# Kernel optimization log

Measured on AMD Instinct MI355X. Metric: run time of the kernel, lower is better.

Reference implementation:

```python
import jax, jax.numpy as jnp
import numpy as np

N = 50000   # nodes
D = 128     # hidden_channels
E = 625000  # edges (before self-loops)
NEG_SLOPE = 0.2


def setup_inputs() -> dict:
    key = jax.random.key(0)
    ks = jax.random.split(key, 10)
    s = 1.0 / np.sqrt(D)
    return {
        "x": jax.random.normal(ks[0], (N, D), dtype=jnp.float32),
        "edge_index": jax.random.randint(ks[1], (2, E), 0, N, dtype=jnp.int64),
        "W1": jax.random.normal(ks[2], (D, D), dtype=jnp.float32) * s,
        "a_src1": jax.random.normal(ks[3], (D,), dtype=jnp.float32) * s,
        "a_dst1": jax.random.normal(ks[4], (D,), dtype=jnp.float32) * s,
        "b1": jax.random.normal(ks[5], (D,), dtype=jnp.float32) * 0.01,
        "W2": jax.random.normal(ks[6], (D, D), dtype=jnp.float32) * s,
        "a_src2": jax.random.normal(ks[7], (D,), dtype=jnp.float32) * s,
        "a_dst2": jax.random.normal(ks[8], (D,), dtype=jnp.float32) * s,
        "b2": jax.random.normal(ks[9], (D,), dtype=jnp.float32) * 0.01,
    }


def gat_layer(x, src, dst, W, a_src, a_dst, b):
    # x: [N, D]; src/dst: [E'] (self-loops already appended)
    h = x @ W                                   # [N, D]
    s_src = h @ a_src                           # [N]
    s_dst = h @ a_dst                           # [N]
    e = s_src[src] + s_dst[dst]                 # [E'] per-edge logits
    e = jnp.where(e > 0, e, NEG_SLOPE * e)      # leaky_relu
    # softmax over incoming edges of each dst node (self-loops -> no empty segments)
    m = jax.ops.segment_max(e, dst, num_segments=N)
    p = jnp.exp(e - m[dst])
    z = jax.ops.segment_sum(p, dst, num_segments=N)
    alpha = p / (z[dst] + 1e-16)                # [E']
    out = jax.ops.segment_sum(alpha[:, None] * h[src], dst, num_segments=N)
    return out + b


def reference(x, edge_index, W1, a_src1, a_dst1, b1, W2, a_src2, a_dst2, b2):
    loop = jnp.arange(N, dtype=edge_index.dtype)
    src = jnp.concatenate([edge_index[0], loop])
    dst = jnp.concatenate([edge_index[1], loop])
    h = jax.nn.relu(gat_layer(x, src, dst, W1, a_src1, a_dst1, b1))
    return gat_layer(h, src, dst, W2, a_src2, a_dst2, b2)
```

## Files before the change

kernel.cpp:

```cpp
#include <hip/hip_runtime.h>
#include <hip/hip_fp16.h>

#define D 128
#define NEG_SLOPE 0.2f


__global__ __launch_bounds__(256) void partial_kernel(const int* __restrict__ deg,
                                                      int* __restrict__ psum, int N) {
  __shared__ int s[256];
  int t = threadIdx.x;
  int i = blockIdx.x * 256 + t;
  s[t] = (i < N) ? deg[i] : 0;
  __syncthreads();
  #pragma unroll
  for (int o = 128; o; o >>= 1) { if (t < o) s[t] += s[t + o]; __syncthreads(); }
  if (t == 0) psum[blockIdx.x] = s[0];
}

__global__ __launch_bounds__(1024) void scan_partials(const int* __restrict__ psum,
                                                      int* __restrict__ bbase,
                                                      int* __restrict__ off, int NB, int N) {
  __shared__ int s[1024];
  int t = threadIdx.x;
  int v = (t < NB) ? psum[t] : 0;
  s[t] = v;
  __syncthreads();
  for (int o = 1; o < 1024; o <<= 1) {
    int u = (t >= o) ? s[t - o] : 0;
    __syncthreads();
    s[t] += u;
    __syncthreads();
  }
  if (t < NB) bbase[t] = s[t] - v;
  if (t == 1023) off[N] = s[1023];
}

__global__ __launch_bounds__(256) void offs_kernel(const int* __restrict__ deg,
                                                   const int* __restrict__ bbase,
                                                   int* __restrict__ off, int N) {
  __shared__ int s[256];
  int t = threadIdx.x;
  int i = blockIdx.x * 256 + t;
  int v = (i < N) ? deg[i] : 0;
  s[t] = v;
  __syncthreads();
  #pragma unroll
  for (int o = 1; o < 256; o <<= 1) {
    int u = (t >= o) ? s[t - o] : 0;
    __syncthreads();
    s[t] += u;
    __syncthreads();
  }
  if (i < N) off[i] = bbase[blockIdx.x] + s[t] - v;
}

__global__ __launch_bounds__(256) void scatter_kernel(
    const int* __restrict__ src, const int* __restrict__ dst,
    const int* __restrict__ rank, int E, int N,
    const int* __restrict__ off, int* __restrict__ csr) {
  int i = blockIdx.x * blockDim.x + threadIdx.x;
  if (i >= E + N) return;
  int s, d;
  if (i < E) { s = src[i]; d = dst[i]; } else { s = i - E; d = s; }
  csr[off[d] + rank[i]] = s;
}


__global__ __launch_bounds__(256, 2) void gemm_hist_fused(
    const float* __restrict__ X, const float* __restrict__ W,
    const float* __restrict__ avs, const float* __restrict__ avd,
    __half* __restrict__ H, float* __restrict__ Ss, float* __restrict__ Sd, int N,
    const int* __restrict__ dstE, int E, int* __restrict__ deg, int* __restrict__ rank,
    int nbGemm, int nbHist)
{
  if (blockIdx.x >= nbGemm) {
    if (dstE == nullptr) return;
    int b = blockIdx.x - nbGemm;
    int EP = E + N;
    int stride = nbHist * 256;
    for (int i = b * 256 + (int)threadIdx.x; i < EP; i += stride) {
      int d = (i < E) ? dstE[i] : (i - E);
      rank[i] = atomicAdd(&deg[d], 1);
    }
    return;
  }

  __shared__ float At[32 * 68];
  __shared__ float Ws[32 * 128];
  int tid = threadIdx.x;
  int tx = tid & 15, ty = tid >> 4;
  int row0 = blockIdx.x * 64;

  float acc[4][8];
  #pragma unroll
  for (int i = 0; i < 4; ++i)
    #pragma unroll
    for (int j = 0; j < 8; ++j) acc[i][j] = 0.f;

  float as_[8], ad_[8];
  #pragma unroll
  for (int j = 0; j < 4; ++j) {
    as_[j]     = avs[tx * 4 + j];      ad_[j]     = avd[tx * 4 + j];
    as_[j + 4] = avs[64 + tx * 4 + j]; ad_[j + 4] = avd[64 + tx * 4 + j];
  }

  for (int kc = 0; kc < 4; ++kc) {
    #pragma unroll
    for (int it = 0; it < 4; ++it) {
      int lin = it * 256 + tid;
      int r = lin >> 4;
      int c2 = lin & 15;
      int gr = row0 + r;
      float2 v = make_float2(0.f, 0.f);
      if (gr < N) v = *(const float2*)&X[(size_t)gr * D + kc * 32 + c2 * 2];
      At[(c2 * 2) * 68 + r] = v.x;
      At[(c2 * 2 + 1) * 68 + r] = v.y;
    }
    #pragma unroll
    for (int it = 0; it < 4; ++it) {
      int lin = it * 256 + tid;
      int r = lin >> 5;
      int c4 = lin & 31;
      *(float4*)&Ws[r * 128 + c4 * 4] =
          *(const float4*)&W[(size_t)(kc * 32 + r) * D + c4 * 4];
    }
    __syncthreads();
    #pragma unroll 8
    for (int k = 0; k < 32; ++k) {
      float4 a0 = *(const float4*)&At[k * 68 + ty * 4];
      float4 w0 = *(const float4*)&Ws[k * 128 + tx * 4];
      float4 w1 = *(const float4*)&Ws[k * 128 + 64 + tx * 4];
      float a[4] = {a0.x, a0.y, a0.z, a0.w};
      float wv[8] = {w0.x, w0.y, w0.z, w0.w, w1.x, w1.y, w1.z, w1.w};
      #pragma unroll
      for (int i = 0; i < 4; ++i)
        #pragma unroll
        for (int j = 0; j < 8; ++j) acc[i][j] += a[i] * wv[j];
    }
    __syncthreads();
  }

  #pragma unroll
  for (int i = 0; i < 4; ++i) {
    int r = row0 + ty * 4 + i;
    bool ok = r < N;
    if (ok) {
      __half2 o0 = __floats2half2_rn(acc[i][0], acc[i][1]);
      __half2 o1 = __floats2half2_rn(acc[i][2], acc[i][3]);
      __half2 o2 = __floats2half2_rn(acc[i][4], acc[i][5]);
      __half2 o3 = __floats2half2_rn(acc[i][6], acc[i][7]);
      *(__half2*)&H[(size_t)r * D + tx * 4]          = o0;
      *(__half2*)&H[(size_t)r * D + tx * 4 + 2]      = o1;
      *(__half2*)&H[(size_t)r * D + 64 + tx * 4]     = o2;
      *(__half2*)&H[(size_t)r * D + 64 + tx * 4 + 2] = o3;
    }
    float ps = 0.f, pd = 0.f;
    #pragma unroll
    for (int j = 0; j < 8; ++j) { ps += acc[i][j] * as_[j]; pd += acc[i][j] * ad_[j]; }
    ps += __shfl_down(ps, 8); pd += __shfl_down(pd, 8);
    ps += __shfl_down(ps, 4); pd += __shfl_down(pd, 4);
    ps += __shfl_down(ps, 2); pd += __shfl_down(pd, 2);
    ps += __shfl_down(ps, 1); pd += __shfl_down(pd, 1);
    if (ok && tx == 0) { Ss[r] = ps; Sd[r] = pd; }
  }
}


__global__ __launch_bounds__(256) void agg_kernel(
    const __half* __restrict__ H, const float* __restrict__ Ssrc, const float* __restrict__ Sdst,
    const int* __restrict__ off, const int* __restrict__ csr, const float* __restrict__ bias,
    float* __restrict__ out, int N, int do_relu)
{
  int wid = threadIdx.x >> 6, lane = threadIdx.x & 63;
  int n = blockIdx.x * 4 + wid;
  if (n >= N) return;
  int st = off[n], en = off[n + 1];
  float sd = Sdst[n];

  float m = -1e30f;
  for (int j = st + lane; j < en; j += 64) {
    int s = csr[j];
    float e = Ssrc[s] + sd;
    e = e > 0.f ? e : NEG_SLOPE * e;
    m = fmaxf(m, e);
  }
  #pragma unroll
  for (int o = 32; o; o >>= 1) m = fmaxf(m, __shfl_xor(m, o));

  float z = 0.f, ax = 0.f, ay = 0.f;
  int c = lane * 2;
  for (int base = st; base < en; base += 64) {
    int j = base + lane;
    int cnt = min(64, en - base);
    float p = 0.f; int s = 0;
    if (j < en) {
      s = csr[j];
      float e = Ssrc[s] + sd;
      e = e > 0.f ? e : NEG_SLOPE * e;
      p = __expf(e - m);
    }
    z += p;
    for (int i = 0; i < cnt; i += 8) {
      float pu[8]; __half2 hv[8];
      #pragma unroll
      for (int u = 0; u < 8; ++u) {
        int idx = i + u;
        int iu = idx < cnt ? idx : cnt - 1;
        float pb = __shfl(p, iu);
        int   sb = __shfl(s, iu);
        pu[u] = idx < cnt ? pb : 0.f;
        hv[u] = *(const __half2*)&H[(size_t)sb * D + c];
      }
      #pragma unroll
      for (int u = 0; u < 8; ++u) {
        float2 f = __half22float2(hv[u]);
        ax += pu[u] * f.x; ay += pu[u] * f.y;
      }
    }
  }
  #pragma unroll
  for (int o = 32; o; o >>= 1) z += __shfl_xor(z, o);
  float inv = 1.f / (z + 1e-16f);
  float2 bv = *(const float2*)&bias[c];
  ax = ax * inv + bv.x;
  ay = ay * inv + bv.y;
  if (do_relu) { ax = fmaxf(ax, 0.f); ay = fmaxf(ay, 0.f); }
  *(float2*)&out[(size_t)n * D + c] = make_float2(ax, ay);
}


extern "C" void kernel_launch(void* const* d_in, const int* in_sizes, int n_in,
                              void* d_out, int out_size, void* d_ws, size_t ws_size,
                              hipStream_t stream) {
  const float* x   = (const float*)d_in[0];
  const int*   ei  = (const int*)d_in[1];
  const float* W1  = (const float*)d_in[2];
  const float* as1 = (const float*)d_in[3];
  const float* ad1 = (const float*)d_in[4];
  const float* b1  = (const float*)d_in[5];
  const float* W2  = (const float*)d_in[6];
  const float* as2 = (const float*)d_in[7];
  const float* ad2 = (const float*)d_in[8];
  const float* b2  = (const float*)d_in[9];

  int N  = in_sizes[0] / D;
  int E  = in_sizes[1] / 2;
  int EP = E + N;
  const int* src = ei;
  const int* dst = ei + E;

  char* w = (char*)d_ws;
  auto alloc = [&](size_t bytes) -> char* {
    char* p = w; w += (bytes + 511) & ~(size_t)511; return p;
  };
  int NB = (N + 255) / 256;
  int*    deg   = (int*)alloc((size_t)N * 4);
  int*    off   = (int*)alloc(((size_t)N + 1) * 4);
  int*    csr   = (int*)alloc((size_t)EP * 4);
  int*    rank  = (int*)alloc((size_t)EP * 4);
  int*    psum  = (int*)alloc((size_t)NB * 4);
  int*    bbase = (int*)alloc((size_t)NB * 4);
  float*  ssrc  = (float*)alloc((size_t)N * 4);
  float*  sdst  = (float*)alloc((size_t)N * 4);
  __half* h     = (__half*)alloc((size_t)N * D * 2);
  float*  t1    = (float*)alloc((size_t)N * D * 4);

  hipMemsetAsync(deg, 0, (size_t)N * 4, stream);

  int nbGemm = (N + 63) / 64;
  int nbHist = 1024;

  gemm_hist_fused<<<nbGemm + nbHist, 256, 0, stream>>>(
      x, W1, as1, ad1, h, ssrc, sdst, N, dst, E, deg, rank, nbGemm, nbHist);

  partial_kernel<<<NB, 256, 0, stream>>>(deg, psum, N);
  scan_partials<<<1, 1024, 0, stream>>>(psum, bbase, off, NB, N);
  offs_kernel<<<NB, 256, 0, stream>>>(deg, bbase, off, N);
  scatter_kernel<<<(EP + 255) / 256, 256, 0, stream>>>(src, dst, rank, E, N, off, csr);

  agg_kernel<<<(N + 3) / 4, 256, 0, stream>>>(h, ssrc, sdst, off, csr, b1, t1, N, 1);
  gemm_hist_fused<<<nbGemm, 256, 0, stream>>>(
      t1, W2, as2, ad2, h, ssrc, sdst, N, nullptr, 0, nullptr, nullptr, nbGemm, 0);
  agg_kernel<<<(N + 3) / 4, 256, 0, stream>>>(h, ssrc, sdst, off, csr, b2, (float*)d_out, N, 0);
}
```

Measured before the change: 244.4 us.

## Use fp16 MFMA for node projection and store intermediate activations in half

Result: no change. 247.3 us (+1.2%).

```diff
diff --git a/kernel.cpp b/kernel.cpp
--- a/kernel.cpp
+++ b/kernel.cpp
@@ -3,6 +3,10 @@
 
 #define D 128
 #define NEG_SLOPE 0.2f
+#define WT_STRIDE 136
+
+typedef __attribute__((ext_vector_type(8))) _Float16 v8h;
+typedef __attribute__((ext_vector_type(4))) float v4f;
 
 
 __global__ __launch_bounds__(256) void partial_kernel(const int* __restrict__ deg,
@@ -67,7 +71,8 @@
 
 
 __global__ __launch_bounds__(256, 2) void gemm_hist_fused(
-    const float* __restrict__ X, const float* __restrict__ W,
+    const float* __restrict__ Xf, const __half* __restrict__ Xh,
+    const float* __restrict__ W,
     const float* __restrict__ avs, const float* __restrict__ avd,
     __half* __restrict__ H, float* __restrict__ Ss, float* __restrict__ Sd, int N,
     const int* __restrict__ dstE, int E, int* __restrict__ deg, int* __restrict__ rank,
@@ -85,83 +90,77 @@
     return;
   }
 
-  __shared__ float At[32 * 68];
-  __shared__ float Ws[32 * 128];
+  __shared__ _Float16 Wt[128][WT_STRIDE];
+  __shared__ _Float16 wa[2][128];
+
   int tid = threadIdx.x;
-  int tx = tid & 15, ty = tid >> 4;
-  int row0 = blockIdx.x * 64;
-
-  float acc[4][8];
-  #pragma unroll
-  for (int i = 0; i < 4; ++i)
+
+  #pragma unroll
+  for (int it = 0; it < 16; ++it) {
+    int lin = it * 256 + tid;
+    int k  = lin >> 5;
+    int n4 = (lin & 31) * 4;
+    float4 v = *(const float4*)&W[(size_t)k * D + n4];
+    Wt[n4 + 0][k] = (_Float16)v.x;
+    Wt[n4 + 1][k] = (_Float16)v.y;
+    Wt[n4 + 2][k] = (_Float16)v.z;
+    Wt[n4 + 3][k] = (_Float16)v.w;
+  }
+  {
+    int k = tid & 127;
+    const float* vec = (tid < 128) ? avs : avd;
+    float s = 0.f;
+    #pragma unroll 8
+    for (int n = 0; n < 128; n += 4) {
+      float4 wv = *(const float4*)&W[(size_t)k * D + n];
+      float4 av = *(const float4*)&vec[n];
+      s += wv.x * av.x + wv.y * av.y + wv.z * av.z + wv.w * av.w;
+    }
+    wa[tid >> 7][k] = (_Float16)s;
+  }
+  __syncthreads();
+
+  int wid = tid >> 6, lane = tid & 63;
+  int quad = lane >> 4, nn = lane & 15;
+  int row = blockIdx.x * 64 + wid * 16 + nn;
+  int rowc = min(row, N - 1);
+
+  v4f acc[9];
+  #pragma unroll
+  for (int t = 0; t < 9; ++t) acc[t] = (v4f){0.f, 0.f, 0.f, 0.f};
+
+  #pragma unroll
+  for (int ks = 0; ks < 4; ++ks) {
+    int k0 = ks * 32 + quad * 8;
+    v8h b;
+    if (Xh) {
+      b = *(const v8h*)&Xh[(size_t)rowc * D + k0];
+    } else {
+      float4 x0 = *(const float4*)&Xf[(size_t)rowc * D + k0];
+      float4 x1 = *(const float4*)&Xf[(size_t)rowc * D + k0 + 4];
+      b[0] = (_Float16)x0.x; b[1] = (_Float16)x0.y;
+      b[2] = (_Float16)x0.z; b[3] = (_Float16)x0.w;
+      b[4] = (_Float16)x1.x; b[5] = (_Float16)x1.y;
+      b[6] = (_Float16)x1.z; b[7] = (_Float16)x1.w;
+    }
     #pragma unroll
-    for (int j = 0; j < 8; ++j) acc[i][j] = 0.f;
-
-  float as_[8], ad_[8];
-  #pragma unroll
-  for (int j = 0; j < 4; ++j) {
-    as_[j]     = avs[tx * 4 + j];      ad_[j]     = avd[tx * 4 + j];
-    as_[j + 4] = avs[64 + tx * 4 + j]; ad_[j + 4] = avd[64 + tx * 4 + j];
-  }
-
-  for (int kc = 0; kc < 4; ++kc) {
+    for (int t = 0; t < 8; ++t) {
+      v8h a = *(const v8h*)&Wt[t * 16 + nn][k0];
+      acc[t] = __builtin_amdgcn_mfma_f32_16x16x32_f16(a, b, acc[t], 0, 0, 0);
+    }
+    v8h awv = *(const v8h*)&wa[nn & 1][k0];
+    acc[8] = __builtin_amdgcn_mfma_f32_16x16x32_f16(awv, b, acc[8], 0, 0, 0);
+  }
+
+  if (row < N) {
     #pragma unroll
-    for (int it = 0; it < 4; ++it) {
-      int lin = it * 256 + tid;
-      int r = lin >> 4;
-      int c2 = lin & 15;
-      int gr = row0 + r;
-      float2 v = make_float2(0.f, 0.f);
-      if (gr < N) v = *(const float2*)&X[(size_t)gr * D + kc * 32 + c2 * 2];
-      At[(c2 * 2) * 68 + r] = v.x;
-      At[(c2 * 2 + 1) * 68 + r] = v.y;
-    }
-    #pragma unroll
-    for (int it = 0; it < 4; ++it) {
-      int lin = it * 256 + tid;
-      int r = lin >> 5;
-      int c4 = lin & 31;
-      *(float4*)&Ws[r * 128 + c4 * 4] =
-          *(const float4*)&W[(size_t)(kc * 32 + r) * D + c4 * 4];
-    }
-    __syncthreads();
-    #pragma unroll 8
-    for (int k = 0; k < 32; ++k) {
-      float4 a0 = *(const float4*)&At[k * 68 + ty * 4];
-      float4 w0 = *(const float4*)&Ws[k * 128 + tx * 4];
-      float4 w1 = *(const float4*)&Ws[k * 128 + 64 + tx * 4];
-      float a[4] = {a0.x, a0.y, a0.z, a0.w};
-      float wv[8] = {w0.x, w0.y, w0.z, w0.w, w1.x, w1.y, w1.z, w1.w};
-      #pragma unroll
-      for (int i = 0; i < 4; ++i)
-        #pragma unroll
-        for (int j = 0; j < 8; ++j) acc[i][j] += a[i] * wv[j];
-    }
-    __syncthreads();
-  }
-
-  #pragma unroll
-  for (int i = 0; i < 4; ++i) {
-    int r = row0 + ty * 4 + i;
-    bool ok = r < N;
-    if (ok) {
-      __half2 o0 = __floats2half2_rn(acc[i][0], acc[i][1]);
-      __half2 o1 = __floats2half2_rn(acc[i][2], acc[i][3]);
-      __half2 o2 = __floats2half2_rn(acc[i][4], acc[i][5]);
-      __half2 o3 = __floats2half2_rn(acc[i][6], acc[i][7]);
-      *(__half2*)&H[(size_t)r * D + tx * 4]          = o0;
-      *(__half2*)&H[(size_t)r * D + tx * 4 + 2]      = o1;
-      *(__half2*)&H[(size_t)r * D + 64 + tx * 4]     = o2;
-      *(__half2*)&H[(size_t)r * D + 64 + tx * 4 + 2] = o3;
-    }
-    float ps = 0.f, pd = 0.f;
-    #pragma unroll
-    for (int j = 0; j < 8; ++j) { ps += acc[i][j] * as_[j]; pd += acc[i][j] * ad_[j]; }
-    ps += __shfl_down(ps, 8); pd += __shfl_down(pd, 8);
-    ps += __shfl_down(ps, 4); pd += __shfl_down(pd, 4);
-    ps += __shfl_down(ps, 2); pd += __shfl_down(pd, 2);
-    ps += __shfl_down(ps, 1); pd += __shfl_down(pd, 1);
-    if (ok && tx == 0) { Ss[r] = ps; Sd[r] = pd; }
+    for (int t = 0; t < 8; ++t) {
+      __half2 h0 = __floats2half2_rn(acc[t].x, acc[t].y);
+      __half2 h1 = __floats2half2_rn(acc[t].z, acc[t].w);
+      *(__half2*)&H[(size_t)row * D + t * 16 + quad * 4]     = h0;
+      *(__half2*)&H[(size_t)row * D + t * 16 + quad * 4 + 2] = h1;
+    }
+    if (quad == 0) { Ss[row] = acc[8].x; Sd[row] = acc[8].y; }
   }
 }
 
@@ -169,7 +168,7 @@
 __global__ __launch_bounds__(256) void agg_kernel(
     const __half* __restrict__ H, const float* __restrict__ Ssrc, const float* __restrict__ Sdst,
     const int* __restrict__ off, const int* __restrict__ csr, const float* __restrict__ bias,
-    float* __restrict__ out, int N, int do_relu)
+    float* __restrict__ outF, __half* __restrict__ outH, int N, int do_relu)
 {
   int wid = threadIdx.x >> 6, lane = threadIdx.x & 63;
   int n = blockIdx.x * 4 + wid;
@@ -225,7 +224,11 @@
   ax = ax * inv + bv.x;
   ay = ay * inv + bv.y;
   if (do_relu) { ax = fmaxf(ax, 0.f); ay = fmaxf(ay, 0.f); }
-  *(float2*)&out[(size_t)n * D + c] = make_float2(ax, ay);
+  if (outH) {
+    *(__half2*)&outH[(size_t)n * D + c] = __floats2half2_rn(ax, ay);
+  } else {
+    *(float2*)&outF[(size_t)n * D + c] = make_float2(ax, ay);
+  }
 }
 
 
@@ -263,7 +266,7 @@
   float*  ssrc  = (float*)alloc((size_t)N * 4);
   float*  sdst  = (float*)alloc((size_t)N * 4);
   __half* h     = (__half*)alloc((size_t)N * D * 2);
-  float*  t1    = (float*)alloc((size_t)N * D * 4);
+  __half* t1h   = (__half*)alloc((size_t)N * D * 2);
 
   hipMemsetAsync(deg, 0, (size_t)N * 4, stream);
 
@@ -271,15 +274,17 @@
   int nbHist = 1024;
 
   gemm_hist_fused<<<nbGemm + nbHist, 256, 0, stream>>>(
-      x, W1, as1, ad1, h, ssrc, sdst, N, dst, E, deg, rank, nbGemm, nbHist);
+      x, nullptr, W1, as1, ad1, h, ssrc, sdst, N, dst, E, deg, rank, nbGemm, nbHist);
 
   partial_kernel<<<NB, 256, 0, stream>>>(deg, psum, N);
   scan_partials<<<1, 1024, 0, stream>>>(psum, bbase, off, NB, N);
   offs_kernel<<<NB, 256, 0, stream>>>(deg, bbase, off, N);
   scatter_kernel<<<(EP + 255) / 256, 256, 0, stream>>>(src, dst, rank, E, N, off, csr);
 
-  agg_kernel<<<(N + 3) / 4, 256, 0, stream>>>(h, ssrc, sdst, off, csr, b1, t1, N, 1);
+  agg_kernel<<<(N + 3) / 4, 256, 0, stream>>>(h, ssrc, sdst, off, csr, b1,
+                                              nullptr, t1h, N, 1);
   gemm_hist_fused<<<nbGemm, 256, 0, stream>>>(
-      t1, W2, as2, ad2, h, ssrc, sdst, N, nullptr, 0, nullptr, nullptr, nbGemm, 0);
-  agg_kernel<<<(N + 3) / 4, 256, 0, stream>>>(h, ssrc, sdst, off, csr, b2, (float*)d_out, N, 0);
-}
+      nullptr, t1h, W2, as2, ad2, h, ssrc, sdst, N, nullptr, 0, nullptr, nullptr, nbGemm, 0);
+  agg_kernel<<<(N + 3) / 4, 256, 0, stream>>>(h, ssrc, sdst, off, csr, b2,
+                                              (float*)d_out, nullptr, N, 0);
+}
```
